# Optimization experiments

Measured on AMD Instinct MI355X. Metric: run time of the kernel, lower is better.

The kernel has to match this reference:

```python
import jax, jax.numpy as jnp
import numpy as np


def setup_inputs() -> dict:
    key = jax.random.key(0)
    k1, k2 = jax.random.split(key)
    queries = jax.random.normal(k1, (8, 4096, 512), dtype=jnp.float32)
    items = jax.random.normal(k2, (1024, 512), dtype=jnp.float32)
    return {"queries": queries, "items": items}


def reference(queries, items):
    # queries: (B, S, F), items: (K, F); reduction='none', memto_framework=True
    # Phase-only (unit magnitude) reconstruction along the sequence axis.
    f = jnp.fft.rfft(queries, axis=1)                     # (B, S//2+1, F) complex64
    unit = jnp.fft.irfft(jnp.exp(-1j * jnp.angle(f)), axis=1)  # (B, S, F) float32 (S even)
    # Dense score against shared memory, then top-1 nearest memory item.
    score = jnp.einsum('bsf,kf->bsk', unit, items)        # (B, S, K)
    idx = jnp.argmax(score, axis=-1)                      # (B, S) int, top-1 index
    step_basis = items[idx]                               # gather -> (B, S, F)
    # MSE with reduction='none' is elementwise squared error; then sum over features.
    gathering_loss = jnp.sum((queries - step_basis) ** 2, axis=-1)  # (B, S)
    return gathering_loss
```

## Files before the change

### kernel.cpp

```cpp
#include <hip/hip_runtime.h>


#define NB 8
#define NS 4096
#define NF 512
#define NK 1024
#define NROWS (NB * NS)
#define NKB 8

#define SWZF(i) ((i) ^ (((i) >> 4) & 15))

typedef _Float16 half8 __attribute__((ext_vector_type(8)));
typedef float floatx4 __attribute__((ext_vector_type(4)));
struct H2 { _Float16 x, y; };

__device__ __forceinline__ float2 cmulf(float2 a, float2 b) {
    return make_float2(a.x * b.x - a.y * b.y, a.x * b.y + a.y * b.x);
}

__device__ __forceinline__ float2 unitize(float2 v) {
    float m2 = v.x * v.x + v.y * v.y;
    if (m2 > 0.f) {
        float inv = 1.0f / sqrtf(m2);
        return make_float2(v.x * inv, v.y * inv);
    }
    return make_float2(1.f, 0.f);
}

__device__ __forceinline__ H2 split_h2(float v) {
    _Float16 h = (_Float16)v;
    float lo = v - (float)h;
    H2 r; r.x = h; r.y = (_Float16)lo; return r;
}

__device__ __forceinline__ void dft4(float2 a, float2 b, float2 c, float2 d,
                                     float2& o0, float2& o1, float2& o2, float2& o3) {
    float2 apc = make_float2(a.x + c.x, a.y + c.y);
    float2 amc = make_float2(a.x - c.x, a.y - c.y);
    float2 bpd = make_float2(b.x + d.x, b.y + d.y);
    float2 bmd = make_float2(b.x - d.x, b.y - d.y);
    o0 = make_float2(apc.x + bpd.x, apc.y + bpd.y);
    o1 = make_float2(amc.x + bmd.y, amc.y - bmd.x);
    o2 = make_float2(apc.x - bpd.x, apc.y - bpd.y);
    o3 = make_float2(amc.x - bmd.y, amc.y + bmd.x);
}

__global__ void twiddle_init(float2* __restrict__ W) {
    int k = blockIdx.x * 256 + threadIdx.x;
    double ang = -2.0 * 3.14159265358979323846 * (double)k / 4096.0;
    W[k] = make_float2((float)cos(ang), (float)sin(ang));
}

__device__ __forceinline__ void fft4096_r16(float2* A, float2* B,
                                            const float2* __restrict__ W, int t) {
    const float C1 = 0.92387953251128674f;
    const float S1 = 0.38268343236508978f;
    const float R2 = 0.70710678118654752f;
    const float2 w1 = make_float2(C1, -S1);
    const float2 w2 = make_float2(R2, -R2);
    const float2 w3 = make_float2(S1, -C1);
    const float2 w4 = make_float2(0.f, -1.f);
    const float2 w6 = make_float2(-R2, -R2);
    const float2 w9 = make_float2(-C1, S1);
#pragma unroll
    for (int st = 0; st < 3; ++st) {
        float2* src = (st == 1) ? B : A;
        float2* dst = (st == 1) ? A : B;
        const int s = (st == 0) ? 1 : (st == 1) ? 16 : 256;
        __syncthreads();
        float2 x[16];
#pragma unroll
        for (int j = 0; j < 16; ++j) x[j] = src[SWZF(t + j * 256)];
        float2 y[4][4];
#pragma unroll
        for (int n0 = 0; n0 < 4; ++n0)
            dft4(x[n0], x[4 + n0], x[8 + n0], x[12 + n0],
                 y[n0][0], y[n0][1], y[n0][2], y[n0][3]);
        y[1][1] = cmulf(w1, y[1][1]);
        y[1][2] = cmulf(w2, y[1][2]);
        y[1][3] = cmulf(w3, y[1][3]);
        y[2][1] = cmulf(w2, y[2][1]);
        y[2][2] = cmulf(w4, y[2][2]);
        y[2][3] = cmulf(w6, y[2][3]);
        y[3][1] = cmulf(w3, y[3][1]);
        y[3][2] = cmulf(w6, y[3][2]);
        y[3][3] = cmulf(w9, y[3][3]);
        float2 z[16];
#pragma unroll
        for (int k0 = 0; k0 < 4; ++k0)
            dft4(y[0][k0], y[1][k0], y[2][k0], y[3][k0],
                 z[k0], z[4 + k0], z[8 + k0], z[12 + k0]);
        const int q = t & (s - 1);
        const int pw = t - q;
        const int dbase = 16 * t - 15 * q;
        dst[SWZF(dbase)] = z[0];
        if (st == 2) {
#pragma unroll
            for (int j = 1; j < 16; ++j)
                dst[SWZF(dbase + j * s)] = z[j];
        } else {
#pragma unroll
            for (int j = 1; j < 16; ++j)
                dst[SWZF(dbase + j * s)] = cmulf(W[(j * pw) & 4095], z[j]);
        }
    }
}

__global__ __launch_bounds__(256) void fft_phase_kernel(
        const float* __restrict__ q, H2* __restrict__ u2,
        const float2* __restrict__ W) {
    __shared__ float2 bufA[4096];
    __shared__ float2 bufB[4096];
    const int t = threadIdx.x;
    const int p = blockIdx.x;
    const int b = p >> 8;
    const int f0 = (p & 255) * 2;
    const float* qb = q + (size_t)b * NS * NF + f0;

#pragma unroll
    for (int i = 0; i < 16; ++i) {
        int s = t + i * 256;
        float2 v = *(const float2*)&qb[(size_t)s * NF];
        bufA[SWZF(s)] = v;
    }

    fft4096_r16(bufA, bufB, W, t);
    __syncthreads();

#pragma unroll
    for (int j = 0; j < 8; ++j) {
        int k = t + j * 256;
        if (k == 0) {
            float2 z0 = bufB[SWZF(0)];
            float2 zh = bufB[SWZF(2048)];
            float2 u00 = unitize(make_float2(z0.x, 0.f));
            float2 u10 = unitize(make_float2(z0.y, 0.f));
            bufB[SWZF(0)] = make_float2(u00.x, u10.x);
            float2 u0h = unitize(make_float2(zh.x, 0.f));
            float2 u1h = unitize(make_float2(zh.y, 0.f));
            bufB[SWZF(2048)] = make_float2(u0h.x, u1h.x);
        } else {
            float2 zk = bufB[SWZF(k)];
            float2 zm = bufB[SWZF(4096 - k)];
            float2 a = make_float2(0.5f * (zk.x + zm.x), 0.5f * (zk.y - zm.y));
            float2 bq = make_float2(0.5f * (zk.x - zm.x), 0.5f * (zk.y + zm.y));
            float2 x1k = make_float2(bq.y, -bq.x);
            float2 u0 = unitize(a);
            float2 u1 = unitize(x1k);
            bufB[SWZF(k)] = make_float2(u0.x - u1.y, u0.y + u1.x);
            bufB[SWZF(4096 - k)] = make_float2(u0.x + u1.y, u1.x - u0.y);
        }
    }

    fft4096_r16(bufB, bufA, W, t);
    __syncthreads();

    H2* o0 = u2 + (size_t)(2 * p) * NS;
    H2* o1 = o0 + NS;
    const float c = 0.25f;
#pragma unroll
    for (int i = 0; i < 4; ++i) {
        int idx = t + i * 256;
        H2 t0[4], t1[4];
#pragma unroll
        for (int k = 0; k < 4; ++k) {
            float2 e = bufA[SWZF(idx * 4 + k)];
            t0[k] = split_h2(e.x * c);
            t1[k] = split_h2(e.y * c);
        }
        *(float4*)&o0[idx * 4] = *(float4*)t0;
        *(float4*)&o1[idx * 4] = *(float4*)t1;
    }
}

__global__ __launch_bounds__(256) void abuild_kernel(
        const H2* __restrict__ u2, _Float16* __restrict__ a3) {
    __shared__ H2 tile[64][65];
    const int b = blockIdx.z;
    const int f0 = blockIdx.y * 64;
    const int s0 = blockIdx.x * 64;
    const int t = threadIdx.x;
    const int fr = t >> 6;
    const int sc = t & 63;
#pragma unroll
    for (int i = 0; i < 16; ++i) {
        int f = fr + i * 4;
        tile[f][sc] = u2[(size_t)(b * NF + f0 + f) * NS + s0 + sc];
    }
    __syncthreads();
    const int s = t >> 2;
    const int qd = t & 3;
    _Float16 xs[16], ys[16];
#pragma unroll
    for (int j = 0; j < 16; ++j) {
        H2 v = tile[qd * 16 + j][s];
        xs[j] = v.x;
        ys[j] = v.y;
    }
    const int f = f0 + qd * 16;
    const int s_g = b * NS + s0 + s;
    const int rb = s_g >> 4;
    const int sl = s_g & 15;
    const int kc = f >> 5;
    const int g0 = (f >> 3) & 3;
    size_t base = ((size_t)rb * 32 + kc) * 512;
    *(float4*)(a3 + base + (g0 * 16 + sl) * 8) = ((float4*)xs)[0];
    *(float4*)(a3 + base + ((g0 + 1) * 16 + sl) * 8) = ((float4*)xs)[1];
    base += 16 * 512;
    *(float4*)(a3 + base + (g0 * 16 + sl) * 8) = ((float4*)ys)[0];
    *(float4*)(a3 + base + ((g0 + 1) * 16 + sl) * 8) = ((float4*)ys)[1];
}

__global__ __launch_bounds__(256) void bbuild_kernel(
        const float* __restrict__ items, _Float16* __restrict__ b3) {
    int id = blockIdx.x * 256 + threadIdx.x;
    int n = id >> 7, fq = id & 127;
    int f = fq * 4;
    float4 v = *(const float4*)&items[(size_t)n * NF + f];
    H2 h0 = split_h2(v.x * 1024.f);
    H2 h1 = split_h2(v.y * 1024.f);
    H2 h2v = split_h2(v.z * 1024.f);
    H2 h3 = split_h2(v.w * 1024.f);
    _Float16 hs[4] = {h0.x, h1.x, h2v.x, h3.x};
    _Float16 ls[4] = {h0.y, h1.y, h2v.y, h3.y};
    const int rb = n >> 4, nl = n & 15;
    const int kc = f >> 5, g = (f >> 3) & 3, off = f & 7;
    size_t base = ((size_t)rb * 32 + kc) * 512 + (g * 16 + nl) * 8 + off;
    *(float2*)(b3 + base) = *(float2*)hs;
    *(float2*)(b3 + base + 16 * 512) = *(float2*)ls;
}

__global__ __launch_bounds__(256, 2) void gemm_mfma_argmax(
        const _Float16* __restrict__ a3, const _Float16* __restrict__ b3,
        float* __restrict__ pbest, int* __restrict__ pidx) {
    __shared__ float smemf[256];
    __shared__ int smemi[256];
    const int id = blockIdx.x;
    const int xcd = id & 7;
    const int j = id >> 3;
    const int kb = j & 7;
    const int sb = xcd * 32 + (j >> 3);
    const int row0 = sb * 128;
    const int n0 = kb * 128;
    const int t = threadIdx.x;
    const int wid = t >> 6, l = t & 63, g = l >> 4, c = l & 15;
    const int wr = wid >> 1, wc = wid & 1;

    floatx4 acc[4][4];
#pragma unroll
    for (int m = 0; m < 4; ++m)
#pragma unroll
        for (int n = 0; n < 4; ++n) acc[m][n] = (floatx4)0.f;

    const _Float16* pa = a3 + ((size_t)(sb * 8 + wr * 4) * 32) * 512 + l * 8;
    const _Float16* pb = b3 + ((size_t)(kb * 8 + wc * 4) * 32) * 512 + l * 8;

    half8 cah[4], cal[4], cbh[4], cbl[4];
    half8 nah[4], nal[4], nbh[4], nbl[4];

#define LOADF(ah, al, bh, bl, ch)                                           \
    {                                                                       \
        _Pragma("unroll") for (int m = 0; m < 4; ++m) {                     \
            ah[m] = *(const half8*)(pa + m * 16384 + (ch) * 512);           \
            al[m] = *(const half8*)(pa + m * 16384 + (16 + (ch)) * 512);    \
        }                                                                   \
        _Pragma("unroll") for (int n = 0; n < 4; ++n) {                     \
            bh[n] = *(const half8*)(pb + n * 16384 + (ch) * 512);           \
            bl[n] = *(const half8*)(pb + n * 16384 + (16 + (ch)) * 512);    \
        }                                                                   \
    }

#define MFMAS(ah, al, bh, bl)                                               \
    {                                                                       \
        _Pragma("unroll") for (int m = 0; m < 4; ++m)                       \
        _Pragma("unroll") for (int n = 0; n < 4; ++n) {                     \
            acc[m][n] = __builtin_amdgcn_mfma_f32_16x16x32_f16(             \
                ah[m], bh[n], acc[m][n], 0, 0, 0);                          \
            acc[m][n] = __builtin_amdgcn_mfma_f32_16x16x32_f16(             \
                al[m], bh[n], acc[m][n], 0, 0, 0);                          \
            acc[m][n] = __builtin_amdgcn_mfma_f32_16x16x32_f16(             \
                ah[m], bl[n], acc[m][n], 0, 0, 0);                          \
        }                                                                   \
    }

    LOADF(cah, cal, cbh, cbl, 0);
    for (int c0 = 0; c0 < 16; c0 += 2) {
        if (c0 + 1 < 16) LOADF(nah, nal, nbh, nbl, c0 + 1);
        MFMAS(cah, cal, cbh, cbl);
        if (c0 + 2 < 16) LOADF(cah, cal, cbh, cbl, c0 + 2);
        MFMAS(nah, nal, nbh, nbl);
    }
#undef LOADF
#undef MFMAS

#pragma unroll
    for (int m = 0; m < 4; ++m) {
#pragma unroll
        for (int rr = 0; rr < 4; ++rr) {
            float best = acc[m][0][rr];
            int bi = c;
#pragma unroll
            for (int n = 1; n < 4; ++n) {
                float v = acc[m][n][rr];
                int ig = n * 16 + c;
                if (v > best) { best = v; bi = ig; }
            }
#pragma unroll
            for (int off = 1; off < 16; off <<= 1) {
                float ov = __shfl_xor(best, off);
                int oi = __shfl_xor(bi, off);
                if (ov > best || (ov == best && oi < bi)) { best = ov; bi = oi; }
            }
            if (c == 0) {
                int s_local = wr * 64 + m * 16 + 4 * g + rr;
                smemf[wc * 128 + s_local] = best;
                smemi[wc * 128 + s_local] = bi;
            }
        }
    }
    __syncthreads();
    if (t < 128) {
        float b0v = smemf[t];
        int b0i = smemi[t];
        float b1v = smemf[128 + t];
        int b1i = smemi[128 + t] + 64;
        float best = b0v; int bi = b0i;
        if (b1v > b0v) { best = b1v; bi = b1i; }
        int row = row0 + t;
        pbest[(size_t)row * NKB + kb] = best;
        pidx[(size_t)row * NKB + kb] = n0 + bi;
    }
}

__global__ __launch_bounds__(256) void combine_loss_kernel(
        const float* __restrict__ q, const float* __restrict__ items,
        const float* __restrict__ pbest, const int* __restrict__ pidx,
        float* __restrict__ out) {
    const int wid = threadIdx.x >> 6;
    const int lane = threadIdx.x & 63;
    const int row = blockIdx.x * 4 + wid;

    float best = pbest[(size_t)row * NKB];
    int bidx = pidx[(size_t)row * NKB];
#pragma unroll
    for (int g = 1; g < NKB; ++g) {
        float v = pbest[(size_t)row * NKB + g];
        if (v > best) { best = v; bidx = pidx[(size_t)row * NKB + g]; }
    }

    const float4* qr = (const float4*)(q + (size_t)row * NF);
    const float4* mr = (const float4*)(items + (size_t)bidx * NF);
    float sum = 0.f;
#pragma unroll
    for (int i = 0; i < 2; ++i) {
        float4 a = qr[lane + i * 64];
        float4 m = mr[lane + i * 64];
        float dx = a.x - m.x, dy = a.y - m.y, dz = a.z - m.z, dw = a.w - m.w;
        sum += dx * dx + dy * dy + dz * dz + dw * dw;
    }
#pragma unroll
    for (int off = 32; off; off >>= 1) sum += __shfl_down(sum, off, 64);
    if (lane == 0) out[row] = sum;
}

extern "C" void kernel_launch(void* const* d_in, const int* in_sizes, int n_in,
                              void* d_out, int out_size, void* d_ws, size_t ws_size,
                              hipStream_t stream) {
    const float* q = (const float*)d_in[0];
    const float* items = (const float*)d_in[1];
    float* out = (float*)d_out;

    char* ws = (char*)d_ws;
    float2* W = (float2*)ws;
    _Float16* a3 = (_Float16*)(ws + 32768);
    H2* u2 = (H2*)(ws + 32768 + (size_t)67108864);
    _Float16* b3 = (_Float16*)(ws + 32768 + (size_t)67108864 * 2);
    float* pbest = (float*)(ws + 32768 + (size_t)67108864 * 2 + 2097152);
    int* pidx = (int*)(ws + 32768 + (size_t)67108864 * 2 + 2097152 + 1048576);

    hipLaunchKernelGGL(twiddle_init, dim3(16), dim3(256), 0, stream, W);
    hipLaunchKernelGGL(fft_phase_kernel, dim3(2048), dim3(256), 0, stream,
                       q, u2, W);
    hipLaunchKernelGGL(abuild_kernel, dim3(64, 8, 8), dim3(256), 0, stream,
                       u2, a3);
    hipLaunchKernelGGL(bbuild_kernel, dim3(512), dim3(256), 0, stream,
                       items, b3);
    hipLaunchKernelGGL(gemm_mfma_argmax, dim3(2048), dim3(256), 0, stream,
                       a3, b3, pbest, pidx);
    hipLaunchKernelGGL(combine_loss_kernel, dim3(NROWS / 4), dim3(256), 0,
                       stream, q, items, pbest, pidx, out);
}
```

Baseline: 332.0 us.

## Make FFT in-place in one LDS buffer and remap block order

```diff
diff --git a/kernel.cpp b/kernel.cpp
--- a/kernel.cpp
+++ b/kernel.cpp
@@ -51,8 +51,9 @@
     W[k] = make_float2((float)cos(ang), (float)sin(ang));
 }
 
-__device__ __forceinline__ void fft4096_r16(float2* A, float2* B,
-                                            const float2* __restrict__ W, int t) {
+__device__ __forceinline__ void fft4096_r16_ip(float2* buf,
+                                               const float2* __restrict__ W,
+                                               int t) {
     const float C1 = 0.92387953251128674f;
     const float S1 = 0.38268343236508978f;
     const float R2 = 0.70710678118654752f;
@@ -64,13 +65,12 @@
     const float2 w9 = make_float2(-C1, S1);
 #pragma unroll
     for (int st = 0; st < 3; ++st) {
-        float2* src = (st == 1) ? B : A;
-        float2* dst = (st == 1) ? A : B;
         const int s = (st == 0) ? 1 : (st == 1) ? 16 : 256;
         __syncthreads();
         float2 x[16];
 #pragma unroll
-        for (int j = 0; j < 16; ++j) x[j] = src[SWZF(t + j * 256)];
+        for (int j = 0; j < 16; ++j) x[j] = buf[SWZF(t + j * 256)];
+        __syncthreads();
         float2 y[4][4];
 #pragma unroll
         for (int n0 = 0; n0 < 4; ++n0)
@@ -93,26 +93,27 @@
         const int q = t & (s - 1);
         const int pw = t - q;
         const int dbase = 16 * t - 15 * q;
-        dst[SWZF(dbase)] = z[0];
+        buf[SWZF(dbase)] = z[0];
         if (st == 2) {
 #pragma unroll
             for (int j = 1; j < 16; ++j)
-                dst[SWZF(dbase + j * s)] = z[j];
+                buf[SWZF(dbase + j * s)] = z[j];
         } else {
 #pragma unroll
             for (int j = 1; j < 16; ++j)
-                dst[SWZF(dbase + j * s)] = cmulf(W[(j * pw) & 4095], z[j]);
+                buf[SWZF(dbase + j * s)] = cmulf(W[(j * pw) & 4095], z[j]);
         }
     }
-}
-
-__global__ __launch_bounds__(256) void fft_phase_kernel(
+    __syncthreads();
+}
+
+__global__ __launch_bounds__(256, 4) void fft_phase_kernel(
         const float* __restrict__ q, H2* __restrict__ u2,
         const float2* __restrict__ W) {
-    __shared__ float2 bufA[4096];
-    __shared__ float2 bufB[4096];
+    __shared__ float2 buf[4096];
     const int t = threadIdx.x;
-    const int p = blockIdx.x;
+    const int id = blockIdx.x;
+    const int p = (id & 7) * 256 + (id >> 3);
     const int b = p >> 8;
     const int f0 = (p & 255) * 2;
     const float* qb = q + (size_t)b * NS * NF + f0;
@@ -121,39 +122,37 @@
     for (int i = 0; i < 16; ++i) {
         int s = t + i * 256;
         float2 v = *(const float2*)&qb[(size_t)s * NF];
-        bufA[SWZF(s)] = v;
-    }
-
-    fft4096_r16(bufA, bufB, W, t);
-    __syncthreads();
+        buf[SWZF(s)] = v;
+    }
+
+    fft4096_r16_ip(buf, W, t);
 
 #pragma unroll
     for (int j = 0; j < 8; ++j) {
         int k = t + j * 256;
         if (k == 0) {
-            float2 z0 = bufB[SWZF(0)];
-            float2 zh = bufB[SWZF(2048)];
+            float2 z0 = buf[SWZF(0)];
+            float2 zh = buf[SWZF(2048)];
             float2 u00 = unitize(make_float2(z0.x, 0.f));
             float2 u10 = unitize(make_float2(z0.y, 0.f));
-            bufB[SWZF(0)] = make_float2(u00.x, u10.x);
+            buf[SWZF(0)] = make_float2(u00.x, u10.x);
             float2 u0h = unitize(make_float2(zh.x, 0.f));
             float2 u1h = unitize(make_float2(zh.y, 0.f));
-            bufB[SWZF(2048)] = make_float2(u0h.x, u1h.x);
+            buf[SWZF(2048)] = make_float2(u0h.x, u1h.x);
         } else {
-            float2 zk = bufB[SWZF(k)];
-            float2 zm = bufB[SWZF(4096 - k)];
+            float2 zk = buf[SWZF(k)];
+            float2 zm = buf[SWZF(4096 - k)];
             float2 a = make_float2(0.5f * (zk.x + zm.x), 0.5f * (zk.y - zm.y));
             float2 bq = make_float2(0.5f * (zk.x - zm.x), 0.5f * (zk.y + zm.y));
             float2 x1k = make_float2(bq.y, -bq.x);
             float2 u0 = unitize(a);
             float2 u1 = unitize(x1k);
-            bufB[SWZF(k)] = make_float2(u0.x - u1.y, u0.y + u1.x);
-            bufB[SWZF(4096 - k)] = make_float2(u0.x + u1.y, u1.x - u0.y);
+            buf[SWZF(k)] = make_float2(u0.x - u1.y, u0.y + u1.x);
+            buf[SWZF(4096 - k)] = make_float2(u0.x + u1.y, u1.x - u0.y);
         }
     }
 
-    fft4096_r16(bufB, bufA, W, t);
-    __syncthreads();
+    fft4096_r16_ip(buf, W, t);
 
     H2* o0 = u2 + (size_t)(2 * p) * NS;
     H2* o1 = o0 + NS;
@@ -164,7 +163,7 @@
         H2 t0[4], t1[4];
 #pragma unroll
         for (int k = 0; k < 4; ++k) {
-            float2 e = bufA[SWZF(idx * 4 + k)];
+            float2 e = buf[SWZF(idx * 4 + k)];
             t0[k] = split_h2(e.x * c);
             t1[k] = split_h2(e.y * c);
         }
```

Result: slower. 371.4 us (+11.9%).
